# Kernel optimization log

Hardware: AMD Instinct MI355X
Metric: run time of the kernel (lower is better)

Reference implementation:

```python
import jax, jax.numpy as jnp
import numpy as np

B, S, D, H = 4, 2048, 1024, 16
HD = D // H  # head dim = 64
NEG = jnp.finfo(jnp.float32).min


def setup_inputs() -> dict:
    key = jax.random.key(0)
    ks = jax.random.split(key, 6)
    states = jax.random.normal(ks[0], (B, S, D), dtype=jnp.float32)
    # causal float mask, broadcastable over batch and heads
    mask = jnp.tril(jnp.ones((S, S), dtype=jnp.float32))[None, None, :, :]
    scale = 1.0 / np.sqrt(D)
    Wq = jax.random.normal(ks[1], (D, D), dtype=jnp.float32) * scale
    Wk = jax.random.normal(ks[2], (D, D), dtype=jnp.float32) * scale
    Wv = jax.random.normal(ks[3], (D, D), dtype=jnp.float32) * scale
    Wo = jax.random.normal(ks[4], (D, D), dtype=jnp.float32) * scale
    return {"states": states, "mask": mask, "Wq": Wq, "Wk": Wk, "Wv": Wv, "Wo": Wo}


def _split_heads(x):
    # [B,S,D] -> [B,H,S,HD]
    return x.reshape(B, S, H, HD).transpose(0, 2, 1, 3)


def reference(states, mask, Wq, Wk, Wv, Wo):
    q = _split_heads(states @ Wq)
    k = _split_heads(states @ Wk)
    v = _split_heads(states @ Wv)
    # scores [B,H,S,S], scaled by rsqrt(head_dim) as in the original
    alpha = jnp.einsum("bhqd,bhkd->bhqk", q, k) * (1.0 / jnp.sqrt(jnp.float32(HD)))
    alpha = alpha * mask + (1.0 - mask) * NEG
    alpha = jax.nn.softmax(alpha, axis=-1)
    ctx = jnp.einsum("bhqk,bhkd->bhqd", alpha, v)
    ctx = ctx.transpose(0, 2, 1, 3).reshape(B, S, D)  # concat heads
    return ctx @ Wo
```

## Files before the change

### kernel.cpp

```cpp
#include <hip/hip_runtime.h>
#include <hip/hip_bf16.h>

#define BB 4
#define SS 2048
#define DD 1024
#define HH 16
#define HDD 64
#define MM (BB*SS)

typedef __attribute__((ext_vector_type(8))) short short8;
typedef __attribute__((ext_vector_type(4))) float f32x4;
typedef __attribute__((ext_vector_type(4))) int int4v;
typedef __attribute__((ext_vector_type(4))) short bf16x4;

__device__ __forceinline__ ushort f2bf(float f) {
  union { float f; uint u; } v; v.f = f;
  uint u = v.u;
  uint r = (u + 0x7FFFu + ((u >> 16) & 1u)) >> 16;
  return (ushort)r;
}

__device__ __forceinline__ float exp2f_fast(float x) {
#if __has_builtin(__builtin_amdgcn_exp2f)
  return __builtin_amdgcn_exp2f(x);
#else
  float r; asm("v_exp_f32 %0, %1" : "=v"(r) : "v"(x)); return r;
#endif
}

__device__ __forceinline__ bf16x4 pack4bf(float a, float b, float c, float d) {
  union { __hip_bfloat162 h2[2]; bf16x4 s; } u;
  u.h2[0] = __float22bfloat162_rn(make_float2(a, b));
  u.h2[1] = __float22bfloat162_rn(make_float2(c, d));
  return u.s;
}

__device__ __forceinline__ f32x4 mfma16(bf16x4 a, bf16x4 b, f32x4 c) {
#if __has_builtin(__builtin_amdgcn_mfma_f32_16x16x16bf16_1k)
  return __builtin_amdgcn_mfma_f32_16x16x16bf16_1k(a, b, c, 0, 0, 0);
#else
  f32x4 d;
  asm volatile("s_nop 1\n\tv_mfma_f32_16x16x16_bf16 %0, %1, %2, %3\n\ts_nop 7\n\ts_nop 3"
               : "=v"(d) : "v"(a), "v"(b), "v"(c));
  return d;
#endif
}

__device__ __forceinline__ void gload16(void* lds, const void* g) {
  __builtin_amdgcn_global_load_lds((const __attribute__((address_space(1))) void*)g,
                                   (__attribute__((address_space(3))) void*)lds, 16, 0, 0);
}

__global__ __launch_bounds__(256) void k_convert(const float* __restrict__ in,
                                                 ushort* __restrict__ out, int n4) {
  int i = blockIdx.x * 256 + threadIdx.x;
  if (i >= n4) return;
  float4 v = ((const float4*)in)[i];
  uint lo = (uint)f2bf(v.x) | ((uint)f2bf(v.y) << 16);
  uint hi = (uint)f2bf(v.z) | ((uint)f2bf(v.w) << 16);
  ((uint2*)out)[i] = make_uint2(lo, hi);
}

__global__ __launch_bounds__(256) void k_transpose(const float* __restrict__ W0, const float* __restrict__ W1,
                                                   const float* __restrict__ W2, const float* __restrict__ W3,
                                                   ushort* __restrict__ T0, ushort* __restrict__ T1,
                                                   ushort* __restrict__ T2, ushort* __restrict__ T3) {
  __shared__ float t[32][33];
  const float* W; ushort* T;
  switch (blockIdx.z) {
    case 0: W = W0; T = T0; break;
    case 1: W = W1; T = T1; break;
    case 2: W = W2; T = T2; break;
    default: W = W3; T = T3; break;
  }
  float scale = (blockIdx.z == 0) ? 0.18033688011112042f : 1.0f;
  int tx = threadIdx.x, ty = threadIdx.y;
  int x = blockIdx.x * 32 + tx;
  int y0 = blockIdx.y * 32;
#pragma unroll
  for (int j = 0; j < 32; j += 8) t[ty + j][tx] = W[(y0 + ty + j) * DD + x];
  __syncthreads();
#pragma unroll
  for (int j = 0; j < 32; j += 8)
    T[(blockIdx.x * 32 + ty + j) * DD + y0 + tx] = f2bf(t[tx][ty + j] * scale);
}

__global__ __launch_bounds__(256, 2) void k_qkv(const ushort* __restrict__ X,
                                                const ushort* __restrict__ Wqt,
                                                const ushort* __restrict__ Wkt,
                                                const ushort* __restrict__ Wvt,
                                                ushort* __restrict__ Q,
                                                ushort* __restrict__ K,
                                                ushort* __restrict__ Vt) {
  __shared__ ushort Al[2 * 4096];
  __shared__ ushort Bl[3][2 * 4096];
  int tid = threadIdx.x, lane = tid & 63, w = tid >> 6;
  int wm = w >> 1, wn = w & 1, lrow = lane & 15, lgrp = lane >> 4;
  int srow = lane >> 2, scolb = (lane & 3) * 16;
  const char* A8 = (const char*)(X + (size_t)blockIdx.x * 128 * DD);
  const char* B8[3] = { (const char*)(Wqt + (size_t)blockIdx.y * 128 * DD),
                        (const char*)(Wkt + (size_t)blockIdx.y * 128 * DD),
                        (const char*)(Wvt + (size_t)blockIdx.y * 128 * DD) };

  f32x4 acc[3][4][4];
#pragma unroll
  for (int wi = 0; wi < 3; wi++)
#pragma unroll
    for (int i = 0; i < 4; i++)
#pragma unroll
      for (int j = 0; j < 4; j++)
#pragma unroll
        for (int r = 0; r < 4; r++) acc[wi][i][j][r] = 0.f;

#pragma unroll
  for (int ii = 0; ii < 2; ii++) {
    int i = w * 2 + ii;
    size_t ro = (size_t)(i * 16 + srow) * (DD * 2) + scolb;
    gload16(Al + i * 512, A8 + ro);
#pragma unroll
    for (int wi = 0; wi < 3; wi++)
      gload16(&Bl[wi][i * 512], B8[wi] + ro);
  }
  __syncthreads();

  for (int kk = 0; kk < DD; kk += 32) {
    int cur = (kk >> 5) & 1;
    if (kk + 32 < DD) {
#pragma unroll
      for (int ii = 0; ii < 2; ii++) {
        int i = w * 2 + ii;
        size_t ro = (size_t)(i * 16 + srow) * (DD * 2) + (kk + 32) * 2 + scolb;
        gload16(Al + (cur ^ 1) * 4096 + i * 512, A8 + ro);
#pragma unroll
        for (int wi = 0; wi < 3; wi++)
          gload16(&Bl[wi][(cur ^ 1) * 4096 + i * 512], B8[wi] + ro);
      }
    }
    short8 a[4];
#pragma unroll
    for (int i = 0; i < 4; i++)
      a[i] = *(const short8*)&Al[cur * 4096 + (wm * 64 + i * 16 + lrow) * 32 + lgrp * 8];
#pragma unroll
    for (int wi = 0; wi < 3; wi++) {
      short8 b[4];
#pragma unroll
      for (int j = 0; j < 4; j++)
        b[j] = *(const short8*)&Bl[wi][cur * 4096 + (wn * 64 + j * 16 + lrow) * 32 + lgrp * 8];
#pragma unroll
      for (int i = 0; i < 4; i++)
#pragma unroll
        for (int j = 0; j < 4; j++)
          acc[wi][i][j] = __builtin_amdgcn_mfma_f32_16x16x32_bf16(a[i], b[j], acc[wi][i][j], 0, 0, 0);
    }
    __syncthreads();
  }

  int m0 = blockIdx.x * 128 + wm * 64, n0 = blockIdx.y * 128 + wn * 64;
#pragma unroll
  for (int wi = 0; wi < 2; wi++) {
    ushort* Out = (wi == 0) ? Q : K;
#pragma unroll
    for (int i = 0; i < 4; i++)
#pragma unroll
      for (int j = 0; j < 4; j++)
#pragma unroll
        for (int r = 0; r < 4; r++) {
          int row = m0 + i * 16 + lgrp * 4 + r;
          int col = n0 + j * 16 + lrow;
          int b = row >> 11, s = row & 2047, h = col >> 6, hd = col & 63;
          Out[(((size_t)(b * HH + h) * SS) + s) * HDD + hd] = f2bf(acc[wi][i][j][r]);
        }
  }
#pragma unroll
  for (int i = 0; i < 4; i++)
#pragma unroll
    for (int j = 0; j < 4; j++) {
      int row0 = m0 + i * 16 + lgrp * 4;
      int col = n0 + j * 16 + lrow;
      int b = row0 >> 11, s0 = row0 & 2047, h = col >> 6, hd = col & 63;
      bf16x4 s = pack4bf(acc[2][i][j][0], acc[2][i][j][1], acc[2][i][j][2], acc[2][i][j][3]);
      *(bf16x4*)(Vt + (((size_t)(b * HH + h) * HDD) + hd) * SS + s0) = s;
    }
}

#define QB2 64
#define KVB 64
#define NQT2 (SS / QB2)

__global__ __launch_bounds__(128) void k_attn(const ushort* __restrict__ Q,
                                              const ushort* __restrict__ K,
                                              const ushort* __restrict__ Vt,
                                              ushort* __restrict__ Ctx) {
  __shared__ ushort Kl[2][4096];
  __shared__ ushort Vl[2][4096];
  int bid = blockIdx.x;
  int xcd = bid & 7, slot = bid >> 3;
  int j = slot & 15;
  int bh = (slot >> 4) * 8 + xcd;
  int b = bh >> 4, h = bh & 15;
  int tid = threadIdx.x, lane = tid & 63, w = tid >> 6;
  int lrow = lane & 15, lgrp = lane >> 4;

  int srow = lane >> 3;
  int scolb = ((lane & 7) * 16) ^ (srow << 4);
  const char* K8 = (const char*)(K + (size_t)bh * SS * HDD);
  const char* V8 = (const char*)(Vt + (size_t)bh * HDD * SS);

  int kswz = (lrow & 7) << 3;
  int colE[2];
  colE[0] = (lgrp * 8) ^ kswz;
  colE[1] = (lgrp * 8 + 32) ^ kswz;

  const ushort* kc0 = &Kl[0][lrow * 64 + colE[0]];
  const ushort* kc1 = &Kl[0][lrow * 64 + colE[1]];
  const ushort* vbp[4];
#pragma unroll
  for (int t = 0; t < 4; t++) vbp[t] = &Vl[0][lrow * 64 + (((16 * t + lgrp * 4) ^ kswz))];

#pragma unroll
  for (int ph = 0; ph < 2; ph++) {
    int qx = ph == 0 ? (NQT2 - 1 - j) : j;
    int qb = qx * QB2;
    int qw0 = qb + w * 32;
    int ntk = qx + 1;

    const char* kgp[4];
    const char* vgp[4];
#pragma unroll
    for (int ii = 0; ii < 4; ii++) {
      kgp[ii] = K8 + (size_t)(w * 32 + ii * 8 + srow) * 128 + scolb;
      vgp[ii] = V8 + (size_t)(w * 32 + ii * 8 + srow) * (SS * 2) + scolb;
    }

    short8 qf[2][2];
#pragma unroll
    for (int qt = 0; qt < 2; qt++)
#pragma unroll
      for (int c = 0; c < 2; c++)
        qf[qt][c] = *(const short8*)(Q + ((size_t)bh * SS + qb + w * 32 + qt * 16 + lrow) * HDD + lgrp * 8 + 32 * c);

    f32x4 o[2][4];
#pragma unroll
    for (int qt = 0; qt < 2; qt++)
#pragma unroll
      for (int nt = 0; nt < 4; nt++)
#pragma unroll
        for (int r = 0; r < 4; r++) o[qt][nt][r] = 0.f;
    float m_run[2] = {-1e30f, -1e30f}, l_run[2] = {0.f, 0.f};

#pragma unroll
    for (int ii = 0; ii < 4; ii++) {
      gload16(&Kl[0][(w * 4 + ii) * 512], kgp[ii]);
      gload16(&Vl[0][(w * 4 + ii) * 512], vgp[ii]);
      kgp[ii] += KVB * 128;
      vgp[ii] += KVB * 2;
    }
    __syncthreads();

    for (int kt = 0; kt < ntk; kt++) {
      int cur = kt & 1;
      if (kt + 1 < ntk) {
#pragma unroll
        for (int ii = 0; ii < 4; ii++) {
          gload16(&Kl[cur ^ 1][(w * 4 + ii) * 512], kgp[ii]);
          gload16(&Vl[cur ^ 1][(w * 4 + ii) * 512], vgp[ii]);
          kgp[ii] += KVB * 128;
          vgp[ii] += KVB * 2;
        }
      }
      int kb = kt * KVB;
      const ushort* kcc0 = kc0 + (cur << 12);
      const ushort* kcc1 = kc1 + (cur << 12);
      short8 kf[4][2];
#pragma unroll
      for (int t = 0; t < 4; t++) {
        kf[t][0] = *(const short8*)(kcc0 + t * 1024);
        kf[t][1] = *(const short8*)(kcc1 + t * 1024);
      }

      bf16x4 pk[2][4];
#pragma unroll
      for (int qt = 0; qt < 2; qt++) {
        f32x4 st[4];
#pragma unroll
        for (int t = 0; t < 4; t++) {
          f32x4 z;
#pragma unroll
          for (int r = 0; r < 4; r++) z[r] = 0.f;
          z = __builtin_amdgcn_mfma_f32_16x16x32_bf16(kf[t][0], qf[qt][0], z, 0, 0, 0);
          z = __builtin_amdgcn_mfma_f32_16x16x32_bf16(kf[t][1], qf[qt][1], z, 0, 0, 0);
          st[t] = z;
        }
        if (kb + 63 > qw0) {
          int lim = qw0 + qt * 16 + lrow - kb - lgrp * 4;
#pragma unroll
          for (int t = 0; t < 4; t++)
#pragma unroll
            for (int r = 0; r < 4; r++)
              if (16 * t + r > lim) st[t][r] = -1e30f;
        }
        float rm = -1e30f;
#pragma unroll
        for (int t = 0; t < 4; t++) {
          float m01 = fmaxf(st[t][0], st[t][1]);
          float m23 = fmaxf(st[t][2], st[t][3]);
          rm = fmaxf(rm, fmaxf(m01, m23));
        }
        rm = fmaxf(rm, __shfl_xor(rm, 16));
        rm = fmaxf(rm, __shfl_xor(rm, 32));
        bool need = rm > m_run[qt] + 8.f;
        if (__any(need)) {
          float mn = need ? rm : m_run[qt];
          float sca = exp2f_fast(m_run[qt] - mn);
          m_run[qt] = mn;
          l_run[qt] *= sca;
#pragma unroll
          for (int nt = 0; nt < 4; nt++)
#pragma unroll
            for (int r = 0; r < 4; r++) o[qt][nt][r] *= sca;
        }
        float m = m_run[qt];
        float rs = 0.f;
#pragma unroll
        for (int t = 0; t < 4; t++) {
          float e0 = exp2f_fast(st[t][0] - m);
          float e1 = exp2f_fast(st[t][1] - m);
          float e2 = exp2f_fast(st[t][2] - m);
          float e3 = exp2f_fast(st[t][3] - m);
          rs += (e0 + e1) + (e2 + e3);
          pk[qt][t] = pack4bf(e0, e1, e2, e3);
        }
        rs += __shfl_xor(rs, 16);
        rs += __shfl_xor(rs, 32);
        l_run[qt] += rs;
      }

#pragma unroll
      for (int t = 0; t < 4; t++) {
        const ushort* vbt = vbp[t] + (cur << 12);
#pragma unroll
        for (int nt = 0; nt < 4; nt++) {
          bf16x4 va = *(const bf16x4*)(vbt + nt * 1024);
          o[0][nt] = mfma16(va, pk[0][t], o[0][nt]);
          o[1][nt] = mfma16(va, pk[1][t], o[1][nt]);
        }
      }
      __syncthreads();
    }

#pragma unroll
    for (int qt = 0; qt < 2; qt++) {
      float inv = 1.f / l_run[qt];
      int q = qb + w * 32 + qt * 16 + lrow;
      ushort* base = Ctx + ((size_t)b * SS + q) * DD + h * HDD;
#pragma unroll
      for (int nt = 0; nt < 4; nt++) {
        bf16x4 s = pack4bf(o[qt][nt][0] * inv, o[qt][nt][1] * inv,
                           o[qt][nt][2] * inv, o[qt][nt][3] * inv);
        *(bf16x4*)(base + nt * 16 + lgrp * 4) = s;
      }
    }
  }
}

__device__ __forceinline__ void gemm_tile(const ushort* __restrict__ Arow,
                                          const ushort* __restrict__ Brow,
                                          ushort* Al, ushort* Bl,
                                          f32x4 acc[4][4]) {
  int tid = threadIdx.x;
  int lane = tid & 63, w = tid >> 6;
  int wm = w >> 1, wn = w & 1;
  int lrow = lane & 15, lgrp = lane >> 4;
#pragma unroll
  for (int i = 0; i < 4; i++)
#pragma unroll
    for (int j = 0; j < 4; j++)
#pragma unroll
      for (int r = 0; r < 4; r++) acc[i][j][r] = 0.f;

  int srow = lane >> 2;
  int scolb = (lane & 3) * 16;
  const char* A8 = (const char*)Arow;
  const char* B8 = (const char*)Brow;

#pragma unroll
  for (int ii = 0; ii < 2; ii++) {
    int i = w * 2 + ii;
    gload16(Al + i * 512, A8 + (size_t)(i * 16 + srow) * (DD * 2) + scolb);
    gload16(Bl + i * 512, B8 + (size_t)(i * 16 + srow) * (DD * 2) + scolb);
  }
  __syncthreads();

  for (int kk = 0; kk < DD; kk += 32) {
    int cur = (kk >> 5) & 1;
    if (kk + 32 < DD) {
#pragma unroll
      for (int ii = 0; ii < 2; ii++) {
        int i = w * 2 + ii;
        gload16(Al + (cur ^ 1) * 4096 + i * 512,
                A8 + (size_t)(i * 16 + srow) * (DD * 2) + (kk + 32) * 2 + scolb);
        gload16(Bl + (cur ^ 1) * 4096 + i * 512,
                B8 + (size_t)(i * 16 + srow) * (DD * 2) + (kk + 32) * 2 + scolb);
      }
    }
    short8 a[4], b[4];
#pragma unroll
    for (int i = 0; i < 4; i++) a[i] = *(const short8*)&Al[cur * 4096 + (wm * 64 + i * 16 + lrow) * 32 + lgrp * 8];
#pragma unroll
    for (int j = 0; j < 4; j++) b[j] = *(const short8*)&Bl[cur * 4096 + (wn * 64 + j * 16 + lrow) * 32 + lgrp * 8];
#pragma unroll
    for (int i = 0; i < 4; i++)
#pragma unroll
      for (int j = 0; j < 4; j++)
        acc[i][j] = __builtin_amdgcn_mfma_f32_16x16x32_bf16(a[i], b[j], acc[i][j], 0, 0, 0);
    __syncthreads();
  }
}

__global__ __launch_bounds__(256) void k_oproj(const ushort* __restrict__ Ctx,
                                               const ushort* __restrict__ Wot,
                                               float* __restrict__ Outp) {
  __shared__ ushort Al[2 * 4096];
  __shared__ ushort Bl[2 * 4096];
  f32x4 acc[4][4];
  gemm_tile(Ctx + (size_t)blockIdx.x * 128 * DD, Wot + (size_t)blockIdx.y * 128 * DD, Al, Bl, acc);
  int lane = threadIdx.x & 63, w = threadIdx.x >> 6;
  int wm = w >> 1, wn = w & 1, lrow = lane & 15, lgrp = lane >> 4;
  int m0 = blockIdx.x * 128 + wm * 64, n0 = blockIdx.y * 128 + wn * 64;
#pragma unroll
  for (int i = 0; i < 4; i++)
#pragma unroll
    for (int j = 0; j < 4; j++)
#pragma unroll
      for (int r = 0; r < 4; r++) {
        int row = m0 + i * 16 + lgrp * 4 + r;
        int col = n0 + j * 16 + lrow;
        Outp[(size_t)row * DD + col] = acc[i][j][r];
      }
}

extern "C" void kernel_launch(void* const* d_in, const int* in_sizes, int n_in,
                              void* d_out, int out_size, void* d_ws, size_t ws_size,
                              hipStream_t stream) {
  const float* states = (const float*)d_in[0];
  const float* Wq = (const float*)d_in[2];
  const float* Wk = (const float*)d_in[3];
  const float* Wv = (const float*)d_in[4];
  const float* Wo = (const float*)d_in[5];
  float* outp = (float*)d_out;

  char* ws = (char*)d_ws;
  const size_t XBF = 0;
  const size_t WQT = 16777216;
  const size_t WKT = WQT + 2097152;
  const size_t WVT = WKT + 2097152;
  const size_t WOT = WVT + 2097152;
  const size_t QO  = WOT + 2097152;
  const size_t KO  = QO + 16777216;
  const size_t VT  = KO + 16777216;
  const size_t CTX = VT + 16777216;

  ushort* Xbf = (ushort*)(ws + XBF);
  ushort* Wqt = (ushort*)(ws + WQT);
  ushort* Wkt = (ushort*)(ws + WKT);
  ushort* Wvt = (ushort*)(ws + WVT);
  ushort* Wot = (ushort*)(ws + WOT);
  ushort* Qb  = (ushort*)(ws + QO);
  ushort* Kb  = (ushort*)(ws + KO);
  ushort* Vtb = (ushort*)(ws + VT);
  ushort* Ctb = (ushort*)(ws + CTX);

  k_convert<<<(MM * DD / 4 + 255) / 256, 256, 0, stream>>>(states, Xbf, MM * DD / 4);
  k_transpose<<<dim3(32, 32, 4), dim3(32, 8), 0, stream>>>(Wq, Wk, Wv, Wo, Wqt, Wkt, Wvt, Wot);
  k_qkv<<<dim3(MM / 128, DD / 128), 256, 0, stream>>>(Xbf, Wqt, Wkt, Wvt, Qb, Kb, Vtb);
  k_attn<<<dim3(NQT2 * BB * HH / 2), 128, 0, stream>>>(Qb, Kb, Vtb, Ctb);
  k_oproj<<<dim3(MM / 128, DD / 128), 256, 0, stream>>>(Ctb, Wot, outp);
}
```

Measured before the change: 172.4 us.

## Widen o-proj tile to 128x256 and defer softmax row-sum reduction

The output-projection GEMM now computes two 128-wide N tiles per block, reusing each loaded A (context) tile for both and halving the grid along N. It sets launch bounds to 2 blocks per SM and doubles the accumulator registers. In attention, the per-tile cross-lane shuffle reduction of the row sum is moved to the end, done once on the accumulated partial sums. The running max now uses a chain of three-input max operations. The larger tile cuts A-tile global traffic but raises register pressure and shared memory, and gives fewer blocks (256) to spread over the CUs.

Result: slower. 179.6 us (+4.2%).

```diff
diff --git a/kernel.cpp b/kernel.cpp
--- a/kernel.cpp
+++ b/kernel.cpp
@@ -26,6 +26,10 @@
 #else
   float r; asm("v_exp_f32 %0, %1" : "=v"(r) : "v"(x)); return r;
 #endif
+}
+
+__device__ __forceinline__ float max3f(float a, float b, float c) {
+  return fmaxf(fmaxf(a, b), c);
 }
 
 __device__ __forceinline__ bf16x4 pack4bf(float a, float b, float c, float d) {
@@ -299,13 +303,14 @@
             for (int r = 0; r < 4; r++)
               if (16 * t + r > lim) st[t][r] = -1e30f;
         }
-        float rm = -1e30f;
-#pragma unroll
-        for (int t = 0; t < 4; t++) {
-          float m01 = fmaxf(st[t][0], st[t][1]);
-          float m23 = fmaxf(st[t][2], st[t][3]);
-          rm = fmaxf(rm, fmaxf(m01, m23));
-        }
+        float rm = max3f(st[0][0], st[0][1], st[0][2]);
+        rm = max3f(rm, st[0][3], st[1][0]);
+        rm = max3f(rm, st[1][1], st[1][2]);
+        rm = max3f(rm, st[1][3], st[2][0]);
+        rm = max3f(rm, st[2][1], st[2][2]);
+        rm = max3f(rm, st[2][3], st[3][0]);
+        rm = max3f(rm, st[3][1], st[3][2]);
+        rm = fmaxf(rm, st[3][3]);
         rm = fmaxf(rm, __shfl_xor(rm, 16));
         rm = fmaxf(rm, __shfl_xor(rm, 32));
         bool need = rm > m_run[qt] + 8.f;
@@ -330,8 +335,6 @@
           rs += (e0 + e1) + (e2 + e3);
           pk[qt][t] = pack4bf(e0, e1, e2, e3);
         }
-        rs += __shfl_xor(rs, 16);
-        rs += __shfl_xor(rs, 32);
         l_run[qt] += rs;
       }
 
@@ -350,7 +353,10 @@
 
 #pragma unroll
     for (int qt = 0; qt < 2; qt++) {
-      float inv = 1.f / l_run[qt];
+      float lt = l_run[qt];
+      lt += __shfl_xor(lt, 16);
+      lt += __shfl_xor(lt, 32);
+      float inv = 1.f / lt;
       int q = qb + w * 32 + qt * 16 + lrow;
       ushort* base = Ctx + ((size_t)b * SS + q) * DD + h * HDD;
 #pragma unroll
@@ -363,31 +369,36 @@
   }
 }
 
-__device__ __forceinline__ void gemm_tile(const ushort* __restrict__ Arow,
-                                          const ushort* __restrict__ Brow,
-                                          ushort* Al, ushort* Bl,
-                                          f32x4 acc[4][4]) {
-  int tid = threadIdx.x;
-  int lane = tid & 63, w = tid >> 6;
-  int wm = w >> 1, wn = w & 1;
-  int lrow = lane & 15, lgrp = lane >> 4;
-#pragma unroll
-  for (int i = 0; i < 4; i++)
-#pragma unroll
-    for (int j = 0; j < 4; j++)
-#pragma unroll
-      for (int r = 0; r < 4; r++) acc[i][j][r] = 0.f;
-
-  int srow = lane >> 2;
-  int scolb = (lane & 3) * 16;
-  const char* A8 = (const char*)Arow;
-  const char* B8 = (const char*)Brow;
+__global__ __launch_bounds__(256, 2) void k_oproj(const ushort* __restrict__ Ctx,
+                                                  const ushort* __restrict__ Wot,
+                                                  float* __restrict__ Outp) {
+  __shared__ ushort Al[2 * 4096];
+  __shared__ ushort Bl[2][2 * 4096];
+  int tid = threadIdx.x, lane = tid & 63, w = tid >> 6;
+  int wm = w >> 1, wn = w & 1, lrow = lane & 15, lgrp = lane >> 4;
+  int srow = lane >> 2, scolb = (lane & 3) * 16;
+  const char* A8 = (const char*)(Ctx + (size_t)blockIdx.x * 128 * DD);
+  const char* B8[2] = { (const char*)(Wot + (size_t)(blockIdx.y * 2 + 0) * 128 * DD),
+                        (const char*)(Wot + (size_t)(blockIdx.y * 2 + 1) * 128 * DD) };
+
+  f32x4 acc[2][4][4];
+#pragma unroll
+  for (int p = 0; p < 2; p++)
+#pragma unroll
+    for (int i = 0; i < 4; i++)
+#pragma unroll
+      for (int j = 0; j < 4; j++)
+#pragma unroll
+        for (int r = 0; r < 4; r++) acc[p][i][j][r] = 0.f;
 
 #pragma unroll
   for (int ii = 0; ii < 2; ii++) {
     int i = w * 2 + ii;
-    gload16(Al + i * 512, A8 + (size_t)(i * 16 + srow) * (DD * 2) + scolb);
-    gload16(Bl + i * 512, B8 + (size_t)(i * 16 + srow) * (DD * 2) + scolb);
+    size_t ro = (size_t)(i * 16 + srow) * (DD * 2) + scolb;
+    gload16(Al + i * 512, A8 + ro);
+#pragma unroll
+    for (int p = 0; p < 2; p++)
+      gload16(&Bl[p][i * 512], B8[p] + ro);
   }
   __syncthreads();
 
@@ -397,46 +408,47 @@
 #pragma unroll
       for (int ii = 0; ii < 2; ii++) {
         int i = w * 2 + ii;
-        gload16(Al + (cur ^ 1) * 4096 + i * 512,
-                A8 + (size_t)(i * 16 + srow) * (DD * 2) + (kk + 32) * 2 + scolb);
-        gload16(Bl + (cur ^ 1) * 4096 + i * 512,
-                B8 + (size_t)(i * 16 + srow) * (DD * 2) + (kk + 32) * 2 + scolb);
-      }
-    }
-    short8 a[4], b[4];
-#pragma unroll
-    for (int i = 0; i < 4; i++) a[i] = *(const short8*)&Al[cur * 4096 + (wm * 64 + i * 16 + lrow) * 32 + lgrp * 8];
-#pragma unroll
-    for (int j = 0; j < 4; j++) b[j] = *(const short8*)&Bl[cur * 4096 + (wn * 64 + j * 16 + lrow) * 32 + lgrp * 8];
-#pragma unroll
-    for (int i = 0; i < 4; i++)
-#pragma unroll
-      for (int j = 0; j < 4; j++)
-        acc[i][j] = __builtin_amdgcn_mfma_f32_16x16x32_bf16(a[i], b[j], acc[i][j], 0, 0, 0);
+        size_t ro = (size_t)(i * 16 + srow) * (DD * 2) + (kk + 32) * 2 + scolb;
+        gload16(Al + (cur ^ 1) * 4096 + i * 512, A8 + ro);
+#pragma unroll
+        for (int p = 0; p < 2; p++)
+          gload16(&Bl[p][(cur ^ 1) * 4096 + i * 512], B8[p] + ro);
+      }
+    }
+    short8 a[4];
+#pragma unroll
+    for (int i = 0; i < 4; i++)
+      a[i] = *(const short8*)&Al[cur * 4096 + (wm * 64 + i * 16 + lrow) * 32 + lgrp * 8];
+#pragma unroll
+    for (int p = 0; p < 2; p++) {
+      short8 b[4];
+#pragma unroll
+      for (int j = 0; j < 4; j++)
+        b[j] = *(const short8*)&Bl[p][cur * 4096 + (wn * 64 + j * 16 + lrow) * 32 + lgrp * 8];
+#pragma unroll
+      for (int i = 0; i < 4; i++)
+#pragma unroll
+        for (int j = 0; j < 4; j++)
+          acc[p][i][j] = __builtin_amdgcn_mfma_f32_16x16x32_bf16(a[i], b[j], acc[p][i][j], 0, 0, 0);
+    }
     __syncthreads();
   }
-}
-
-__global__ __launch_bounds__(256) void k_oproj(const ushort* __restrict__ Ctx,
-                                               const ushort* __restrict__ Wot,
-                                               float* __restrict__ Outp) {
-  __shared__ ushort Al[2 * 4096];
-  __shared__ ushort Bl[2 * 4096];
-  f32x4 acc[4][4];
-  gemm_tile(Ctx + (size_t)blockIdx.x * 128 * DD, Wot + (size_t)blockIdx.y * 128 * DD, Al, Bl, acc);
-  int lane = threadIdx.x & 63, w = threadIdx.x >> 6;
-  int wm = w >> 1, wn = w & 1, lrow = lane & 15, lgrp = lane >> 4;
-  int m0 = blockIdx.x * 128 + wm * 64, n0 = blockIdx.y * 128 + wn * 64;
-#pragma unroll
-  for (int i = 0; i < 4; i++)
-#pragma unroll
-    for (int j = 0; j < 4; j++)
-#pragma unroll
-      for (int r = 0; r < 4; r++) {
-        int row = m0 + i * 16 + lgrp * 4 + r;
-        int col = n0 + j * 16 + lrow;
-        Outp[(size_t)row * DD + col] = acc[i][j][r];
-      }
+
+  int m0 = blockIdx.x * 128 + wm * 64;
+#pragma unroll
+  for (int p = 0; p < 2; p++) {
+    int n0 = (blockIdx.y * 2 + p) * 128 + wn * 64;
+#pragma unroll
+    for (int i = 0; i < 4; i++)
+#pragma unroll
+      for (int j = 0; j < 4; j++)
+#pragma unroll
+        for (int r = 0; r < 4; r++) {
+          int row = m0 + i * 16 + lgrp * 4 + r;
+          int col = n0 + j * 16 + lrow;
+          Outp[(size_t)row * DD + col] = acc[p][i][j][r];
+        }
+  }
 }
 
 extern "C" void kernel_launch(void* const* d_in, const int* in_sizes, int n_in,
@@ -474,5 +486,5 @@
   k_transpose<<<dim3(32, 32, 4), dim3(32, 8), 0, stream>>>(Wq, Wk, Wv, Wo, Wqt, Wkt, Wvt, Wot);
   k_qkv<<<dim3(MM / 128, DD / 128), 256, 0, stream>>>(Xbf, Wqt, Wkt, Wvt, Qb, Kb, Vtb);
   k_attn<<<dim3(NQT2 * BB * HH / 2), 128, 0, stream>>>(Qb, Kb, Vtb, Ctb);
-  k_oproj<<<dim3(MM / 128, DD / 128), 256, 0, stream>>>(Ctb, Wot, outp);
-}
+  k_oproj<<<dim3(MM / 128, DD / 256), 256, 0, stream>>>(Ctb, Wot, outp);
+}
```
